# Kernel tuning notes

Measured on AMD Instinct MI355X. Metric: run time of the kernel, lower is better.

Reference implementation:

```python
import jax, jax.numpy as jnp
import numpy as np

B, J = 131072, 24
# SMPL skeleton parent indices (root = joint 0)
SMPL_PARENTS = np.array([-1, 0, 0, 0, 1, 2, 3, 4, 5, 6, 7, 8, 9, 9, 9, 12, 13, 14, 16, 17, 18, 19, 20, 21], dtype=np.int64)


def setup_inputs() -> dict:
    key = jax.random.key(0)
    k1, k2 = jax.random.split(key)
    positions = jax.random.normal(k1, (B, J, 3), dtype=jnp.float32)
    rotations = jax.random.normal(k2, (B, J, 4), dtype=jnp.float32)
    return {"parents": SMPL_PARENTS, "positions": positions, "rotations": rotations}


def _quat_to_rotmat(q):
    # q: [B, J, 4] (w, x, y, z); normalize then standard unit-quaternion rotation matrix
    q = q / jnp.linalg.norm(q, axis=-1, keepdims=True)
    qw, qx, qy, qz = q[..., 0], q[..., 1], q[..., 2], q[..., 3]
    x2, y2, z2 = qx + qx, qy + qy, qz + qz
    xx, yy, zz = qx * x2, qy * y2, qz * z2
    xy, yz, xz = qx * y2, qy * z2, qx * z2
    wx, wy, wz = qw * x2, qw * y2, qw * z2
    row0 = jnp.stack([1.0 - (yy + zz), xy - wz, xz + wy], axis=-1)
    row1 = jnp.stack([xy + wz, 1.0 - (xx + zz), yz - wx], axis=-1)
    row2 = jnp.stack([xz - wy, yz + wx, 1.0 - (xx + yy)], axis=-1)
    return jnp.stack([row0, row1, row2], axis=-2)  # [B, J, 3, 3]


def _local_transforms(positions, rotations):
    R = _quat_to_rotmat(rotations)                       # [B, J, 3, 3]
    top = jnp.concatenate([R, positions[..., None]], axis=-1)  # [B, J, 3, 4]
    bottom = jnp.broadcast_to(
        jnp.array([0.0, 0.0, 0.0, 1.0], dtype=rotations.dtype), top.shape[:2] + (1, 4))
    return jnp.concatenate([top, bottom], axis=-2)       # [B, J, 4, 4]


def reference(parents, positions, rotations):
    parents = np.asarray(parents)  # static skeleton topology
    locals_ = _local_transforms(positions, rotations)    # [B, J, 4, 4]
    n_joints = parents.shape[0]
    # Sequential parent-child chain over the (small, static) joint tree.
    g = [locals_[:, 0]]
    for jt in range(1, n_joints):
        g.append(jnp.matmul(g[int(parents[jt])], locals_[:, jt]))
    globals_ = jnp.stack(g, axis=1)                      # [B, J, 4, 4]
    p = globals_[:, :, :, 3]                             # homogeneous positions [B, J, 4]
    return p[:, :, :3] / p[:, :, 3:4]                    # [B, J, 3]
```

## Files before the change

### kernel.cpp

```cpp
#include <hip/hip_runtime.h>


typedef float f32x4 __attribute__((ext_vector_type(4)));

struct M { float r0,r1,r2,r3,r4,r5,r6,r7,r8,tx,ty,tz; };

__device__ __forceinline__ M loc(float a, float b, float c, float d,
                                 float px, float py, float pz) {
    float inv = rsqrtf(a*a + b*b + c*c + d*d);
    float qw = a*inv, qx = b*inv, qy = c*inv, qz = d*inv;
    float x2 = qx+qx, y2 = qy+qy, z2 = qz+qz;
    float xx = qx*x2, yy = qy*y2, zz = qz*z2;
    float xy = qx*y2, yz = qy*z2, xz = qx*z2;
    float wx = qw*x2, wy = qw*y2, wz = qw*z2;
    M m;
    m.r0 = 1.f-(yy+zz); m.r1 = xy-wz;       m.r2 = xz+wy;
    m.r3 = xy+wz;       m.r4 = 1.f-(xx+zz); m.r5 = yz-wx;
    m.r6 = xz-wy;       m.r7 = yz+wx;       m.r8 = 1.f-(xx+yy);
    m.tx = px; m.ty = py; m.tz = pz;
    return m;
}

__device__ __forceinline__ M mul(const M& a, const M& b) {
    M c;
    c.r0 = a.r0*b.r0 + a.r1*b.r3 + a.r2*b.r6;
    c.r1 = a.r0*b.r1 + a.r1*b.r4 + a.r2*b.r7;
    c.r2 = a.r0*b.r2 + a.r1*b.r5 + a.r2*b.r8;
    c.r3 = a.r3*b.r0 + a.r4*b.r3 + a.r5*b.r6;
    c.r4 = a.r3*b.r1 + a.r4*b.r4 + a.r5*b.r7;
    c.r5 = a.r3*b.r2 + a.r4*b.r5 + a.r5*b.r8;
    c.r6 = a.r6*b.r0 + a.r7*b.r3 + a.r8*b.r6;
    c.r7 = a.r6*b.r1 + a.r7*b.r4 + a.r8*b.r7;
    c.r8 = a.r6*b.r2 + a.r7*b.r5 + a.r8*b.r8;
    c.tx = a.r0*b.tx + a.r1*b.ty + a.r2*b.tz + a.tx;
    c.ty = a.r3*b.tx + a.r4*b.ty + a.r5*b.tz + a.ty;
    c.tz = a.r6*b.tx + a.r7*b.ty + a.r8*b.tz + a.tz;
    return c;
}

#define SPB    64
#define NTHR   512
#define GRIDP  256
#define RPITCH 100
#define PPITCH 73

constexpr int MT0[6]  = {0,1,2,4,7,10};
constexpr int PR0[6]  = {-1,0,0,1,3,4};
constexpr int MT1[8]  = {0,2,5,8,11,3,6,9};
constexpr int PR1[8]  = {-1,0,1,2,3,0,5,6};
constexpr int MT2[11] = {0,3,6,9,12,15,13,16,18,20,22};
constexpr int PR2[11] = {-1,0,1,2,3,4,3,6,7,8,9};
constexpr int MT3[9]  = {0,3,6,9,14,17,19,21,23};
constexpr int PR3[9]  = {-1,0,1,2,3,4,5,6,7};

template<int NM>
__device__ __forceinline__ void run_chain(const int (&MT)[NM], const int (&PR)[NM],
                                          int WS,
                                          const float* __restrict__ R,
                                          const float* __restrict__ P,
                                          float* __restrict__ O) {
    M G[NM];
    {
        f32x4 q = *(const f32x4*)(R);
        G[0] = loc(q.x, q.y, q.z, q.w, P[0], P[1], P[2]);
    }
    if (WS == 0) { O[0]=G[0].tx; O[1]=G[0].ty; O[2]=G[0].tz; }
#pragma unroll
    for (int k = 1; k < NM; ++k) {
        const int j = MT[k];
        f32x4 q = *(const f32x4*)(R + 4*j);
        M L = loc(q.x, q.y, q.z, q.w, P[3*j], P[3*j+1], P[3*j+2]);
        G[k] = mul(G[PR[k]], L);
        if (k >= WS) { O[3*j]=G[k].tx; O[3*j+1]=G[k].ty; O[3*j+2]=G[k].tz; }
    }
}

__device__ __forceinline__ void load_regs(int c, int mt,
                                          const float* __restrict__ rot,
                                          const float* __restrict__ pos,
                                          size_t limR, size_t limP,
                                          f32x4 (&vr)[6], f32x4 (&vp)[5]) {
    const size_t baseR = (size_t)c * (SPB*96);
    const size_t baseP = (size_t)c * (SPB*72);
#pragma unroll
    for (int i = 0; i < 6; ++i) {
        const size_t gi = baseR + (size_t)(i*1024 + 4*mt);
        f32x4 v = {0.f,0.f,0.f,0.f};
        if (gi < limR) v = *(const f32x4*)(rot + gi);
        vr[i] = v;
    }
#pragma unroll
    for (int i = 0; i < 5; ++i) {
        const bool g = (i < 4) || (mt < 128);
        const size_t gi = baseP + (size_t)(i*1024 + 4*mt);
        f32x4 v = {0.f,0.f,0.f,0.f};
        if (g && gi < limP) v = *(const f32x4*)(pos + gi);
        vp[i] = v;
    }
}

__device__ __forceinline__ void scatter_lds(int mt,
                                            float* __restrict__ Rb,
                                            float* __restrict__ Pb,
                                            const f32x4 (&vr)[6],
                                            const f32x4 (&vp)[5]) {
#pragma unroll
    for (int i = 0; i < 6; ++i) {
        const int f = i*1024 + 4*mt;
        const int s = f / 96, r = f - 96*s;
        *(f32x4*)(Rb + s*RPITCH + r) = vr[i];
    }
#pragma unroll
    for (int i = 0; i < 5; ++i) {
        if ((i < 4) || (mt < 128)) {
            const int f = i*1024 + 4*mt;
            const int s = f / 72, r = f - 72*s;
            float* d = Pb + s*PPITCH + r;
            d[0]=vp[i].x; d[1]=vp[i].y; d[2]=vp[i].z; d[3]=vp[i].w;
        }
    }
}

__device__ __forceinline__ void store_chunk(const float* __restrict__ Ob,
                                            int c, int mt, size_t limP,
                                            float* __restrict__ out) {
    const size_t baseO = (size_t)c * (SPB*72);
#pragma unroll
    for (int n = 0; n < 5; ++n) {
        if ((n < 4) || (mt < 128)) {
            const int F = n*1024 + 4*mt;
            const int s = F / 72, r = F - 72*s;
            const size_t gi = baseO + (size_t)F;
            if (gi < limP) {
                f32x4 v = { Ob[s*PPITCH+r+0], Ob[s*PPITCH+r+1],
                            Ob[s*PPITCH+r+2], Ob[s*PPITCH+r+3] };
                *(f32x4*)(out + gi) = v;
            }
        }
    }
}

__global__ __launch_bounds__(NTHR, 2) void fk_kernel(
    const float* __restrict__ rot,
    const float* __restrict__ pos,
    float*       __restrict__ out,
    int B)
{
    __shared__ __align__(16) float ldsR[2][SPB * RPITCH];
    __shared__ float ldsP[2][SPB * PPITCH];
    __shared__ float ldsO[2][SPB * PPITCH];

    const int t   = threadIdx.x;
    const int w   = t >> 6;
    const bool cw = (w < 4);
    const int mt  = t & 255;
    const int nch = (B + SPB - 1) / SPB;
    const size_t limR = (size_t)B * 96;
    const size_t limP = (size_t)B * 72;

    const int c0 = blockIdx.x;
    if (!cw && c0 < nch) {
        f32x4 vr[6], vp[5];
        load_regs(c0, mt, rot, pos, limR, limP, vr, vp);
        scatter_lds(mt, ldsR[0], ldsP[0], vr, vp);
    }
    __syncthreads();

    int i = 0, c = c0;
    for (; c < nch; c += GRIDP, ++i) {
        const int q = i & 1;
        if (cw) {
            const int l = t & 63;
            const int b = c * SPB + l;
            if (b < B) {
                const float* R = &ldsR[q][l * RPITCH];
                const float* P = &ldsP[q][l * PPITCH];
                float*       O = &ldsO[q][l * PPITCH];
                switch (w) {
                    case 0:  run_chain(MT0, PR0, 0, R, P, O); break;
                    case 1:  run_chain(MT1, PR1, 2, R, P, O); break;
                    case 2:  run_chain(MT2, PR2, 4, R, P, O); break;
                    default: run_chain(MT3, PR3, 4, R, P, O); break;
                }
            }
        } else {
            const int cn = c + GRIDP;
            const bool ldv = (cn < nch);
            f32x4 vr[6], vp[5];
            if (ldv) load_regs(cn, mt, rot, pos, limR, limP, vr, vp);
            if (i > 0) store_chunk(ldsO[q^1], c - GRIDP, mt, limP, out);
            if (ldv) scatter_lds(mt, ldsR[q^1], ldsP[q^1], vr, vp);
        }
        __syncthreads();
    }

    if (!cw && i > 0)
        store_chunk(ldsO[(i-1) & 1], c - GRIDP, mt, limP, out);
}

extern "C" void kernel_launch(void* const* d_in, const int* in_sizes, int n_in,
                              void* d_out, int out_size, void* d_ws, size_t ws_size,
                              hipStream_t stream) {
    const int B = out_size / 72;
    const void* rot = nullptr;
    const void* pos = nullptr;
    for (int i = 0; i < n_in; ++i) {
        if      (in_sizes[i] == B * 96) rot = d_in[i];
        else if (in_sizes[i] == B * 72) pos = d_in[i];
    }
    if (!rot) rot = d_in[2];
    if (!pos) pos = d_in[1];

    const int nch  = (B + SPB - 1) / SPB;
    const int grid = (nch < GRIDP) ? nch : GRIDP;
    fk_kernel<<<grid, NTHR, 0, stream>>>(
        (const float*)rot, (const float*)pos, (float*)d_out, B);
}
```

Before: 125.4 us.

## Prefetch two chunks ahead in registers and use lightweight LDS-only barriers

Loader waves now keep two register sets and prefetch global data two chunks ahead, unrolling the loop by two so the sets alternate. Global loads get more time in flight before they are scattered to LDS. The __syncthreads is replaced by an lgkmcnt(0) wait plus s_barrier, which avoids waiting on outstanding vector memory loads at each barrier. Launch bounds drop to one block per SIMD group to make room for the extra registers, which may reduce occupancy.

```diff
diff --git a/kernel.cpp b/kernel.cpp
--- a/kernel.cpp
+++ b/kernel.cpp
@@ -140,7 +140,12 @@
     }
 }
 
-__global__ __launch_bounds__(NTHR, 2) void fk_kernel(
+__device__ __forceinline__ void lgkm_fence_barrier() {
+    asm volatile("s_waitcnt lgkmcnt(0)" ::: "memory");
+    __builtin_amdgcn_s_barrier();
+}
+
+__global__ __launch_bounds__(NTHR, 1) void fk_kernel(
     const float* __restrict__ rot,
     const float* __restrict__ pos,
     float*       __restrict__ out,
@@ -157,45 +162,62 @@
     const int nch = (B + SPB - 1) / SPB;
     const size_t limR = (size_t)B * 96;
     const size_t limP = (size_t)B * 72;
-
-    const int c0 = blockIdx.x;
-    if (!cw && c0 < nch) {
-        f32x4 vr[6], vp[5];
-        load_regs(c0, mt, rot, pos, limR, limP, vr, vp);
-        scatter_lds(mt, ldsR[0], ldsP[0], vr, vp);
-    }
-    __syncthreads();
-
-    int i = 0, c = c0;
-    for (; c < nch; c += GRIDP, ++i) {
-        const int q = i & 1;
-        if (cw) {
-            const int l = t & 63;
-            const int b = c * SPB + l;
-            if (b < B) {
-                const float* R = &ldsR[q][l * RPITCH];
-                const float* P = &ldsP[q][l * PPITCH];
-                float*       O = &ldsO[q][l * PPITCH];
-                switch (w) {
-                    case 0:  run_chain(MT0, PR0, 0, R, P, O); break;
-                    case 1:  run_chain(MT1, PR1, 2, R, P, O); break;
-                    case 2:  run_chain(MT2, PR2, 4, R, P, O); break;
-                    default: run_chain(MT3, PR3, 4, R, P, O); break;
-                }
-            }
-        } else {
-            const int cn = c + GRIDP;
-            const bool ldv = (cn < nch);
-            f32x4 vr[6], vp[5];
-            if (ldv) load_regs(cn, mt, rot, pos, limR, limP, vr, vp);
-            if (i > 0) store_chunk(ldsO[q^1], c - GRIDP, mt, limP, out);
-            if (ldv) scatter_lds(mt, ldsR[q^1], ldsP[q^1], vr, vp);
+    const int c0  = blockIdx.x;
+
+    f32x4 vrA[6], vpA[5];
+    f32x4 vrB[6], vpB[5];
+
+    if (!cw) {
+        if (c0 < nch) {
+            load_regs(c0, mt, rot, pos, limR, limP, vrB, vpB);
+            scatter_lds(mt, ldsR[0], ldsP[0], vrB, vpB);
         }
-        __syncthreads();
-    }
-
-    if (!cw && i > 0)
-        store_chunk(ldsO[(i-1) & 1], c - GRIDP, mt, limP, out);
+        if (c0 + GRIDP < nch)
+            load_regs(c0 + GRIDP, mt, rot, pos, limR, limP, vrA, vpA);
+    }
+    lgkm_fence_barrier();
+
+#define FK_GEN(c_, Q_, VRP, VPP, VRN, VPN)                                   \
+    {                                                                        \
+        if (cw) {                                                            \
+            const int l = t & 63;                                            \
+            const int b = (c_) * SPB + l;                                    \
+            if (b < B) {                                                     \
+                const float* R = &ldsR[Q_][l * RPITCH];                      \
+                const float* P = &ldsP[Q_][l * PPITCH];                      \
+                float*       O = &ldsO[Q_][l * PPITCH];                      \
+                switch (w) {                                                 \
+                    case 0:  run_chain(MT0, PR0, 0, R, P, O); break;         \
+                    case 1:  run_chain(MT1, PR1, 2, R, P, O); break;         \
+                    case 2:  run_chain(MT2, PR2, 4, R, P, O); break;         \
+                    default: run_chain(MT3, PR3, 4, R, P, O); break;         \
+                }                                                            \
+            }                                                                \
+        } else {                                                             \
+            if ((c_) + 2*GRIDP < nch)                                        \
+                load_regs((c_) + 2*GRIDP, mt, rot, pos, limR, limP, VRN, VPN);\
+            if ((c_) > c0)                                                   \
+                store_chunk(ldsO[(Q_)^1], (c_) - GRIDP, mt, limP, out);      \
+            if ((c_) + GRIDP < nch)                                          \
+                scatter_lds(mt, ldsR[(Q_)^1], ldsP[(Q_)^1], VRP, VPP);       \
+        }                                                                    \
+        lgkm_fence_barrier();                                                \
+    }
+
+    int c = c0;
+    while (c < nch) {
+        FK_GEN(c, 0, vrA, vpA, vrB, vpB);
+        c += GRIDP;
+        if (c >= nch) break;
+        FK_GEN(c, 1, vrB, vpB, vrA, vpA);
+        c += GRIDP;
+    }
+#undef FK_GEN
+
+    if (!cw && c > c0) {
+        const int lastq = (((c - c0) / GRIDP) - 1) & 1;
+        store_chunk(ldsO[lastq], c - GRIDP, mt, limP, out);
+    }
 }
 
 extern "C" void kernel_launch(void* const* d_in, const int* in_sizes, int n_in,
```

New measurement: 135.7 us. 1.08x slower.
